# Kernel tuning notes

Measured on AMD Instinct MI355X. Metric: run time of the kernel, lower is better.

The kernel has to match this reference:

```python
import jax, jax.numpy as jnp
import numpy as np

N, B, C, K, FF = 1024, 8, 256, 4, 2048

def layer_norm(x, g, b, eps=1e-5):
    mu = jnp.mean(x, axis=-1, keepdims=True)
    var = jnp.var(x, axis=-1, keepdims=True)
    return (x - mu) / jnp.sqrt(var + eps) * g + b

def setup_inputs() -> dict:
    key = jax.random.key(0)
    ks = jax.random.split(key, 10)
    s = 0.02
    return {
        "src_tokens": jax.random.normal(ks[0], (N, B, C), jnp.float32),
        "matched_token_list": jax.random.normal(ks[1], (K, N, B, C), jnp.float32),
        "pos_embed": jax.random.normal(ks[2], (N, B, C), jnp.float32),
        "mask": jnp.zeros((B, N, N), jnp.float32),
        "W_agg": jax.random.normal(ks[3], (C * K, C), jnp.float32) * s,
        "b_agg": jnp.zeros((C,), jnp.float32),
        "W1": jax.random.normal(ks[4], (C, FF), jnp.float32) * s,
        "b1": jnp.zeros((FF,), jnp.float32),
        "W2": jax.random.normal(ks[5], (FF, C), jnp.float32) * s,
        "b2": jnp.zeros((C,), jnp.float32),
        "g1": jnp.ones((C,), jnp.float32),
        "be1": jnp.zeros((C,), jnp.float32),
        "g2": jnp.ones((C,), jnp.float32),
        "be2": jnp.zeros((C,), jnp.float32),
    }

def reference(src_tokens, matched_token_list, pos_embed, mask,
              W_agg, b_agg, W1, b1, W2, b2, g1, be1, g2, be2):
    # q: (n,b,c) -> (b,n,c); k/v: (K,n,b,c) -> (K,b,n,c)
    q = jnp.transpose(src_tokens + pos_embed, (1, 0, 2))
    k = jnp.transpose(matched_token_list + pos_embed[None], (0, 2, 1, 3))
    v = jnp.transpose(matched_token_list, (0, 2, 1, 3))
    q_scaled = q / jnp.sqrt(jnp.asarray(q.shape[-1], q.dtype))
    # scores: (K,b,n,n) with additive mask bias
    scores = jnp.einsum('bnc,kbmc->kbnm', q_scaled, k) + mask[None]
    attn = jax.nn.softmax(scores, axis=-1)
    out_k = jnp.einsum('kbnm,kbmc->kbnc', attn, v)  # (K,b,n,c)
    # concat over K on channel dim: (b,n,K*c)
    cat = jnp.transpose(out_k, (1, 2, 0, 3)).reshape(q.shape[0], q.shape[1], -1)
    rec = cat @ W_agg + b_agg  # (b,n,c)
    rec = jnp.transpose(rec, (1, 0, 2))  # (n,b,c)
    rec = layer_norm(src_tokens + rec, g1, be1)
    ffn = jax.nn.relu(rec @ W1 + b1) @ W2 + b2
    rec = layer_norm(rec + ffn, g2, be2)
    return rec
```

## Files before the change

### kernel.cpp

```cpp
#include <hip/hip_runtime.h>

#define N_SEQ 1024
#define B_SZ 8
#define C_DIM 256
#define K_HEADS 4
#define FF_DIM 2048

typedef short s16x8 __attribute__((ext_vector_type(8)));
typedef float f32x4v __attribute__((ext_vector_type(4)));

#define GLOAD_LDS16(src, dst)                                                              \
    __builtin_amdgcn_global_load_lds((const __attribute__((address_space(1))) void*)(src), \
                                     (__attribute__((address_space(3))) void*)(dst), 16, 0, 0)

__device__ __forceinline__ unsigned short f2bf(float f) {
    unsigned u = __builtin_bit_cast(unsigned, f);
    u += 0x7FFFu + ((u >> 16) & 1u);
    return (unsigned short)(u >> 16);
}
__device__ __forceinline__ float bf2f(unsigned short h) {
    unsigned u = ((unsigned)h) << 16;
    return __builtin_bit_cast(float, u);
}


__global__ __launch_bounds__(256) void prep_q_kernel(const float* __restrict__ src,
                                                     const float* __restrict__ pos,
                                                     unsigned short* __restrict__ qb) {
    int t = blockIdx.x * 256 + threadIdx.x;
    int i4 = t * 4;
    float4 s = *reinterpret_cast<const float4*>(src + i4);
    float4 p = *reinterpret_cast<const float4*>(pos + i4);
    int n = i4 >> 11;
    int rem = i4 & 2047;
    int b = rem >> 8;
    int c = rem & 255;
    int out = (b * N_SEQ + n) * C_DIM + c;
    *reinterpret_cast<ushort4*>(qb + out) = make_ushort4(
        f2bf((s.x + p.x) * 0.0625f), f2bf((s.y + p.y) * 0.0625f),
        f2bf((s.z + p.z) * 0.0625f), f2bf((s.w + p.w) * 0.0625f));
}

__global__ __launch_bounds__(256) void prep_kv_kernel(const float* __restrict__ matched,
                                                      const float* __restrict__ pos,
                                                      unsigned short* __restrict__ kb,
                                                      unsigned short* __restrict__ vfrag) {
    __shared__ unsigned short Vl[64][256];
    int blk = blockIdx.x;
    int nt = blk & 15, pr = blk >> 4;
    int k = pr >> 3, b = pr & 7;
    int n0 = nt * 64;
    int t = threadIdx.x;
    int c4 = (t & 63) * 4;
#pragma unroll
    for (int r = 0; r < 16; r++) {
        int nl = (t >> 6) * 16 + r;
        int n = n0 + nl;
        size_t mi = ((size_t)(k * N_SEQ + n) * B_SZ + b) * C_DIM + c4;
        float4 m = *reinterpret_cast<const float4*>(matched + mi);
        float4 p = *reinterpret_cast<const float4*>(pos + ((size_t)n * B_SZ + b) * C_DIM + c4);
        *reinterpret_cast<ushort4*>(kb + ((size_t)pr * N_SEQ + n) * C_DIM + c4) =
            make_ushort4(f2bf(m.x + p.x), f2bf(m.y + p.y), f2bf(m.z + p.z), f2bf(m.w + p.w));
        *reinterpret_cast<ushort4*>(&Vl[nl][c4]) =
            make_ushort4(f2bf(m.x), f2bf(m.y), f2bf(m.z), f2bf(m.w));
    }
    __syncthreads();
#pragma unroll
    for (int h = 0; h < 2; h++) {
        unsigned short* tb = vfrag + ((size_t)(pr * 32 + nt * 2 + h)) * 8192;
#pragma unroll
        for (int g = 0; g < 4; g++) {
            int c2 = t + 256 * g;
            int ct = c2 >> 6;
            int lane2 = c2 & 63;
            int l152 = lane2 & 15, lg2 = lane2 >> 4;
            s16x8 v;
#pragma unroll
            for (int e = 0; e < 8; e++)
                v[e] = (short)Vl[h * 32 + lg2 * 8 + e][ct * 16 + l152];
            *reinterpret_cast<s16x8*>(tb + (size_t)c2 * 8) = v;
        }
    }
}

__global__ __launch_bounds__(256) void transpose_all_kernel(const float* __restrict__ Wagg,
                                                            const float* __restrict__ W1,
                                                            const float* __restrict__ W2,
                                                            unsigned short* __restrict__ WaggT,
                                                            unsigned short* __restrict__ W1T,
                                                            unsigned short* __restrict__ W2T) {
    int idx = blockIdx.x * 256 + threadIdx.x;
    if (idx < 262144) {
        int c = idx >> 10, r = idx & 1023;
        WaggT[idx] = f2bf(Wagg[(size_t)r * 256 + c]);
    } else if (idx < 786432) {
        int i = idx - 262144;
        int c = i >> 8, r = i & 255;
        W1T[i] = f2bf(W1[(size_t)r * 2048 + c]);
    } else {
        int i = idx - 786432;
        int c = i >> 11, r = i & 2047;
        W2T[i] = f2bf(W2[(size_t)r * 256 + c]);
    }
}

__global__ __launch_bounds__(256, 2) void attn_kernel(const unsigned short* __restrict__ qb,
                                                      const unsigned short* __restrict__ kb,
                                                      const unsigned short* __restrict__ vfrag,
                                                      const float* __restrict__ mask,
                                                      unsigned short* __restrict__ att) {
    __shared__ unsigned short Kl[2][8192];
    __shared__ unsigned short Psh[2][4][16][40];
    __shared__ float scl[2][4][17];
    __shared__ float lrex[4][17];

    int bx = blockIdx.x;
    int b = bx & 7;
    int r2 = bx >> 3;
    int kidx = r2 & 3;
    int qtb = r2 >> 2;
    int pr = kidx * 8 + b;

    int tid = threadIdx.x, wid = tid >> 6, lane = tid & 63;
    int l15 = lane & 15, lg = lane >> 4;
    int q0 = qtb * 64 + wid * 16;

    s16x8 qf[8];
    const unsigned short* qrow = qb + ((size_t)(b * N_SEQ + q0 + l15)) * C_DIM + lg * 8;
#pragma unroll
    for (int cc = 0; cc < 8; cc++) qf[cc] = *reinterpret_cast<const s16x8*>(qrow + cc * 32);

    f32x4v oacc[16];
#pragma unroll
    for (int i = 0; i < 16; i++) oacc[i] = (f32x4v){0.f, 0.f, 0.f, 0.f};
    float mrun = -3e38f, lrun = 0.f;

    const unsigned short* kbp = kb + (size_t)pr * N_SEQ * C_DIM;
    const unsigned short* vfp = vfrag + (size_t)pr * 32 * 8192 + lane * 8;
    const float* mrow = mask + ((size_t)b * N_SEQ + q0 + l15) * N_SEQ;

    auto stage_k = [&](int kv0, unsigned short* buf) {
#pragma unroll
        for (int i = 0; i < 4; i++) {
            int ch = (wid * 4 + i) * 64 + lane;
            int r = ch >> 5;
            int ce = ((ch & 31) * 8) ^ ((r & 7) << 3);
            GLOAD_LDS16(kbp + (size_t)(kv0 + r) * C_DIM + ce, &buf[(wid * 4 + i) * 512]);
        }
    };

    stage_k(0, &Kl[0][0]);
    f32x4v mc0 = *reinterpret_cast<const f32x4v*>(mrow + lg * 4);
    f32x4v mc1 = *reinterpret_cast<const f32x4v*>(mrow + 16 + lg * 4);

    int swz = (l15 & 7) << 3;
    for (int t = 0; t < 32; t++) {
        int cur = t & 1;
        int kv0 = t * 32;
        __syncthreads();
        if (t + 1 < 32) stage_k(kv0 + 32, &Kl[cur ^ 1][0]);

        const unsigned short* vsrc = vfp + (size_t)t * 8192;
        s16x8 vreg[4];
#pragma unroll
        for (int c = 0; c < 4; c++)
            vreg[c] = *reinterpret_cast<const s16x8*>(vsrc + (wid * 4 + c) * 512);

        f32x4v s0 = {0.f, 0.f, 0.f, 0.f}, s1 = {0.f, 0.f, 0.f, 0.f};
        const unsigned short* KlB = &Kl[cur][0];
        __builtin_amdgcn_s_setprio(1);
#pragma unroll
        for (int cc = 0; cc < 8; cc++) {
            s16x8 k0 = *reinterpret_cast<const s16x8*>(KlB + l15 * 256 + ((cc * 32 + lg * 8) ^ swz));
            s16x8 k1 = *reinterpret_cast<const s16x8*>(KlB + (16 + l15) * 256 + ((cc * 32 + lg * 8) ^ swz));
            s0 = __builtin_amdgcn_mfma_f32_16x16x32_bf16(k0, qf[cc], s0, 0, 0, 0);
            s1 = __builtin_amdgcn_mfma_f32_16x16x32_bf16(k1, qf[cc], s1, 0, 0, 0);
        }
        __builtin_amdgcn_s_setprio(0);
#pragma unroll
        for (int jj = 0; jj < 4; jj++) { s0[jj] += mc0[jj]; s1[jj] += mc1[jj]; }
        if (t + 1 < 32) {
            mc0 = *reinterpret_cast<const f32x4v*>(mrow + kv0 + 32 + lg * 4);
            mc1 = *reinterpret_cast<const f32x4v*>(mrow + kv0 + 48 + lg * 4);
        }

        float pm = fmaxf(fmaxf(fmaxf(s0[0], s0[1]), fmaxf(s0[2], s0[3])),
                         fmaxf(fmaxf(s1[0], s1[1]), fmaxf(s1[2], s1[3])));
        pm = fmaxf(pm, __shfl_xor(pm, 16));
        pm = fmaxf(pm, __shfl_xor(pm, 32));
        float sc = 1.0f;
        if (__any(pm > mrun + 8.f)) {
            float mn = fmaxf(mrun, pm);
            sc = __expf(mrun - mn);
            mrun = mn;
        }
        float p0[4], p1[4];
#pragma unroll
        for (int jj = 0; jj < 4; jj++) {
            p0[jj] = __expf(s0[jj] - mrun);
            p1[jj] = __expf(s1[jj] - mrun);
        }
        float ps = (p0[0] + p0[1]) + (p0[2] + p0[3]) + (p1[0] + p1[1]) + (p1[2] + p1[3]);
        ps += __shfl_xor(ps, 16);
        ps += __shfl_xor(ps, 32);
        lrun = lrun * sc + ps;

        *reinterpret_cast<ushort4*>(&Psh[cur][wid][l15][lg * 4]) =
            make_ushort4(f2bf(p0[0]), f2bf(p0[1]), f2bf(p0[2]), f2bf(p0[3]));
        *reinterpret_cast<ushort4*>(&Psh[cur][wid][l15][16 + lg * 4]) =
            make_ushort4(f2bf(p1[0]), f2bf(p1[1]), f2bf(p1[2]), f2bf(p1[3]));
        if (lane < 16) scl[cur][wid][lane] = sc;
        __syncthreads();

        __builtin_amdgcn_s_setprio(1);
#pragma unroll
        for (int j = 0; j < 4; j++) {
            float scj = scl[cur][j][l15];
            s16x8 pf = *reinterpret_cast<const s16x8*>(&Psh[cur][j][l15][lg * 8]);
            if (__any(scj != 1.0f)) {
#pragma unroll
                for (int c = 0; c < 4; c++)
#pragma unroll
                    for (int jj = 0; jj < 4; jj++) oacc[j * 4 + c][jj] *= scj;
            }
#pragma unroll
            for (int c = 0; c < 4; c++) {
                int idx = j * 4 + c;
                oacc[idx] = __builtin_amdgcn_mfma_f32_16x16x32_bf16(vreg[c], pf, oacc[idx], 0, 0, 0);
            }
        }
        __builtin_amdgcn_s_setprio(0);
    }

    if (lane < 16) lrex[wid][lane] = lrun;
    __syncthreads();
#pragma unroll
    for (int j = 0; j < 4; j++) {
        float invj = 1.0f / lrex[j][l15];
#pragma unroll
        for (int c = 0; c < 4; c++) {
            int idx = j * 4 + c;
            size_t orow = ((size_t)(b * N_SEQ + qtb * 64 + j * 16 + l15)) * (K_HEADS * C_DIM)
                          + kidx * C_DIM + wid * 64 + c * 16 + lg * 4;
            *reinterpret_cast<ushort4*>(att + orow) =
                make_ushort4(f2bf(oacc[idx][0] * invj), f2bf(oacc[idx][1] * invj),
                             f2bf(oacc[idx][2] * invj), f2bf(oacc[idx][3] * invj));
        }
    }
}

template <int BM, int BN, int RELU, int OUTBF, int SPLITK>
__global__ __launch_bounds__(256) void gemm_bt_kernel(const unsigned short* __restrict__ A,
                                                      const unsigned short* __restrict__ Bt,
                                                      const float* __restrict__ bias,
                                                      float* __restrict__ Cf0,
                                                      float* __restrict__ Cf1,
                                                      unsigned short* __restrict__ Cb,
                                                      int M, int Nn, int Kd) {
    constexpr int WAVES_N = (BM == 128) ? 2 : 4;
    constexpr int WN = BN / WAVES_N;
    constexpr int NT = WN / 16;
    constexpr int TILE = (BM + BN) * 64;
    constexpr int CALLS = (BM + BN) / 32;
    __shared__ unsigned short Sl[2][TILE];
    int tm0 = blockIdx.y * BM, tn0 = blockIdx.x * BN;
    int kz = (SPLITK == 2) ? blockIdx.z : 0;
    int kbase = kz * (Kd / SPLITK);
    int tid = threadIdx.x, wid = tid >> 6, lane = tid & 63;
    int l15 = lane & 15, lg = lane >> 4;
    int wm = (wid / WAVES_N) * 64, wn = (wid % WAVES_N) * WN;

    f32x4v acc[4][NT];
#pragma unroll
    for (int i = 0; i < 4; i++)
#pragma unroll
        for (int j = 0; j < NT; j++) acc[i][j] = (f32x4v){0.f, 0.f, 0.f, 0.f};

    auto stage = [&](int k0, unsigned short* buf) {
#pragma unroll
        for (int i = 0; i < CALLS; i++) {
            int chb = (i * 4 + wid) * 64;
            int ch = chb + lane;
            const unsigned short* src;
            if (chb < BM * 8) {
                int r = ch >> 3;
                int c8 = ((ch & 7) * 8) ^ ((r & 7) << 3);
                src = A + (size_t)(tm0 + r) * Kd + k0 + c8;
            } else {
                int ch2 = ch - BM * 8;
                int r = ch2 >> 3;
                int c8 = ((ch2 & 7) * 8) ^ ((r & 7) << 3);
                src = Bt + (size_t)(tn0 + r) * Kd + k0 + c8;
            }
            GLOAD_LDS16(src, buf + chb * 8);
        }
    };

    stage(kbase, &Sl[0][0]);
    int nk = (Kd / SPLITK) >> 6;
    int swz = (l15 & 7) << 3;
    for (int kt = 0; kt < nk; kt++) {
        int cur = kt & 1;
        __syncthreads();
        if (kt + 1 < nk) stage(kbase + (kt + 1) * 64, &Sl[cur ^ 1][0]);
        const unsigned short* SA = &Sl[cur][0];
        const unsigned short* SB = SA + BM * 64;
        s16x8 af[4][2], bf[NT][2];
#pragma unroll
        for (int mt = 0; mt < 4; mt++)
#pragma unroll
            for (int h = 0; h < 2; h++)
                af[mt][h] = *reinterpret_cast<const s16x8*>(
                    SA + (wm + mt * 16 + l15) * 64 + ((h * 32 + lg * 8) ^ swz));
#pragma unroll
        for (int nt = 0; nt < NT; nt++)
#pragma unroll
            for (int h = 0; h < 2; h++)
                bf[nt][h] = *reinterpret_cast<const s16x8*>(
                    SB + (wn + nt * 16 + l15) * 64 + ((h * 32 + lg * 8) ^ swz));
        __builtin_amdgcn_s_setprio(1);
#pragma unroll
        for (int mt = 0; mt < 4; mt++)
#pragma unroll
            for (int nt = 0; nt < NT; nt++) {
                acc[mt][nt] = __builtin_amdgcn_mfma_f32_16x16x32_bf16(af[mt][0], bf[nt][0], acc[mt][nt], 0, 0, 0);
                acc[mt][nt] = __builtin_amdgcn_mfma_f32_16x16x32_bf16(af[mt][1], bf[nt][1], acc[mt][nt], 0, 0, 0);
            }
        __builtin_amdgcn_s_setprio(0);
    }

    float* Cf = (SPLITK == 2 && kz) ? Cf1 : Cf0;
#pragma unroll
    for (int mt = 0; mt < 4; mt++) {
#pragma unroll
        for (int nt = 0; nt < NT; nt++) {
#pragma unroll
            for (int j = 0; j < 4; j++) {
                int row = tm0 + wm + mt * 16 + lg * 4 + j;
                int col = tn0 + wn + nt * 16 + l15;
                float bv = (SPLITK == 2 && kz) ? 0.f : bias[col];
                float v = acc[mt][nt][j] + bv;
                if (RELU) v = fmaxf(v, 0.f);
                if (OUTBF) Cb[(size_t)row * Nn + col] = f2bf(v);
                else       Cf[(size_t)row * Nn + col] = v;
            }
        }
    }
}

__global__ __launch_bounds__(256) void ln1_kernel(const float* __restrict__ src,
                                                  const float* __restrict__ p0,
                                                  const float* __restrict__ p1,
                                                  const float* __restrict__ g,
                                                  const float* __restrict__ be,
                                                  unsigned short* __restrict__ outb) {
    int r = blockIdx.x * 4 + (threadIdx.x >> 6);
    int lane = threadIdx.x & 63;
    int n = r >> 3, b = r & 7;
    int c = lane * 4;
    size_t tb_ = ((size_t)(b * N_SEQ + n)) * C_DIM + c;
    float4 xs = *reinterpret_cast<const float4*>(src + (size_t)r * C_DIM + c);
    float4 xa = *reinterpret_cast<const float4*>(p0 + tb_);
    float4 xb = *reinterpret_cast<const float4*>(p1 + tb_);
    float x[4] = {xs.x + xa.x + xb.x, xs.y + xa.y + xb.y,
                  xs.z + xa.z + xb.z, xs.w + xa.w + xb.w};
    float s = x[0] + x[1] + x[2] + x[3];
    float q = x[0] * x[0] + x[1] * x[1] + x[2] * x[2] + x[3] * x[3];
#pragma unroll
    for (int d = 1; d < 64; d <<= 1) {
        s += __shfl_xor(s, d);
        q += __shfl_xor(q, d);
    }
    float mean = s * (1.f / 256.f);
    float var = q * (1.f / 256.f) - mean * mean;
    float rstd = rsqrtf(var + 1e-5f);
    float4 gv = *reinterpret_cast<const float4*>(g + c);
    float4 bv = *reinterpret_cast<const float4*>(be + c);
    *reinterpret_cast<ushort4*>(outb + (size_t)r * C_DIM + c) = make_ushort4(
        f2bf((x[0] - mean) * rstd * gv.x + bv.x), f2bf((x[1] - mean) * rstd * gv.y + bv.y),
        f2bf((x[2] - mean) * rstd * gv.z + bv.z), f2bf((x[3] - mean) * rstd * gv.w + bv.w));
}

__global__ __launch_bounds__(256) void ln2_kernel(const unsigned short* __restrict__ rec1b,
                                                  const float* __restrict__ p0,
                                                  const float* __restrict__ p1,
                                                  const float* __restrict__ g,
                                                  const float* __restrict__ be,
                                                  float* __restrict__ out) {
    int r = blockIdx.x * 4 + (threadIdx.x >> 6);
    int lane = threadIdx.x & 63;
    int c = lane * 4;
    size_t base = (size_t)r * C_DIM + c;
    ushort4 xr = *reinterpret_cast<const ushort4*>(rec1b + base);
    float4 xa = *reinterpret_cast<const float4*>(p0 + base);
    float4 xb = *reinterpret_cast<const float4*>(p1 + base);
    float x[4] = {bf2f(xr.x) + xa.x + xb.x, bf2f(xr.y) + xa.y + xb.y,
                  bf2f(xr.z) + xa.z + xb.z, bf2f(xr.w) + xa.w + xb.w};
    float s = x[0] + x[1] + x[2] + x[3];
    float q = x[0] * x[0] + x[1] * x[1] + x[2] * x[2] + x[3] * x[3];
#pragma unroll
    for (int d = 1; d < 64; d <<= 1) {
        s += __shfl_xor(s, d);
        q += __shfl_xor(q, d);
    }
    float mean = s * (1.f / 256.f);
    float var = q * (1.f / 256.f) - mean * mean;
    float rstd = rsqrtf(var + 1e-5f);
    float4 gv = *reinterpret_cast<const float4*>(g + c);
    float4 bv = *reinterpret_cast<const float4*>(be + c);
    *reinterpret_cast<float4*>(out + base) = make_float4(
        (x[0] - mean) * rstd * gv.x + bv.x,
        (x[1] - mean) * rstd * gv.y + bv.y,
        (x[2] - mean) * rstd * gv.z + bv.z,
        (x[3] - mean) * rstd * gv.w + bv.w);
}


extern "C" void kernel_launch(void* const* d_in, const int* in_sizes, int n_in,
                              void* d_out, int out_size, void* d_ws, size_t ws_size,
                              hipStream_t stream) {
    const float* src   = (const float*)d_in[0];
    const float* match = (const float*)d_in[1];
    const float* pos   = (const float*)d_in[2];
    const float* mask  = (const float*)d_in[3];
    const float* Wagg  = (const float*)d_in[4];
    const float* bagg  = (const float*)d_in[5];
    const float* W1    = (const float*)d_in[6];
    const float* b1    = (const float*)d_in[7];
    const float* W2    = (const float*)d_in[8];
    const float* b2    = (const float*)d_in[9];
    const float* g1    = (const float*)d_in[10];
    const float* be1   = (const float*)d_in[11];
    const float* g2    = (const float*)d_in[12];
    const float* be2   = (const float*)d_in[13];

    char* ws = (char*)d_ws;
    unsigned short* qb    = (unsigned short*)(ws + 0);
    unsigned short* kb    = (unsigned short*)(ws + 4194304);
    unsigned short* vfrag = (unsigned short*)(ws + 20971520);
    unsigned short* att   = (unsigned short*)(ws + 37748736);
    unsigned short* WaggT = (unsigned short*)(ws + 54525952);
    unsigned short* W1T   = (unsigned short*)(ws + 55050240);
    unsigned short* W2T   = (unsigned short*)(ws + 56098816);
    float*          rec_p0 = (float*)(ws + 57147392);
    float*          rec_p1 = (float*)(ws + 65536000);
    unsigned short* rec1b = (unsigned short*)(ws + 0);
    unsigned short* hid   = (unsigned short*)(ws + 4194304);
    float*          ffn_p0 = rec_p0;
    float*          ffn_p1 = rec_p1;
    float* outp = (float*)d_out;

    prep_q_kernel<<<2048, 256, 0, stream>>>(src, pos, qb);
    prep_kv_kernel<<<512, 256, 0, stream>>>(match, pos, kb, vfrag);
    transpose_all_kernel<<<5120, 256, 0, stream>>>(Wagg, W1, W2, WaggT, W1T, W2T);

    attn_kernel<<<512, 256, 0, stream>>>(qb, kb, vfrag, mask, att);

    gemm_bt_kernel<64, 128, 0, 0, 2><<<dim3(2, 128, 2), 256, 0, stream>>>(
        att, WaggT, bagg, rec_p0, rec_p1, nullptr, B_SZ * N_SEQ, C_DIM, K_HEADS * C_DIM);
    ln1_kernel<<<2048, 256, 0, stream>>>(src, rec_p0, rec_p1, g1, be1, rec1b);
    gemm_bt_kernel<128, 128, 1, 1, 1><<<dim3(16, 64), 256, 0, stream>>>(
        rec1b, W1T, b1, nullptr, nullptr, hid, N_SEQ * B_SZ, FF_DIM, C_DIM);
    gemm_bt_kernel<64, 128, 0, 0, 2><<<dim3(2, 128, 2), 256, 0, stream>>>(
        hid, W2T, b2, ffn_p0, ffn_p1, nullptr, N_SEQ * B_SZ, C_DIM, FF_DIM);
    ln2_kernel<<<2048, 256, 0, stream>>>(rec1b, ffn_p0, ffn_p1, g2, be2, outp);
}
```

Baseline: 145.1 us.

## Split attention KV range across two blocks and merge with a combine kernel

```diff
diff --git a/kernel.cpp b/kernel.cpp
--- a/kernel.cpp
+++ b/kernel.cpp
@@ -104,26 +104,30 @@
     }
 }
 
-__global__ __launch_bounds__(256, 2) void attn_kernel(const unsigned short* __restrict__ qb,
+__global__ __launch_bounds__(256, 4) void attn_kernel(const unsigned short* __restrict__ qb,
                                                       const unsigned short* __restrict__ kb,
                                                       const unsigned short* __restrict__ vfrag,
                                                       const float* __restrict__ mask,
-                                                      unsigned short* __restrict__ att) {
+                                                      unsigned short* __restrict__ op0,
+                                                      unsigned short* __restrict__ op1,
+                                                      float2* __restrict__ mlb) {
     __shared__ unsigned short Kl[2][8192];
-    __shared__ unsigned short Psh[2][4][16][40];
-    __shared__ float scl[2][4][17];
+    __shared__ unsigned short Psh[4][16][40];
+    __shared__ float scl[4][17];
     __shared__ float lrex[4][17];
 
     int bx = blockIdx.x;
     int b = bx & 7;
     int r2 = bx >> 3;
-    int kidx = r2 & 3;
-    int qtb = r2 >> 2;
+    int half = r2 & 1;
+    int kidx = (r2 >> 1) & 3;
+    int qtb = r2 >> 3;
     int pr = kidx * 8 + b;
 
     int tid = threadIdx.x, wid = tid >> 6, lane = tid & 63;
     int l15 = lane & 15, lg = lane >> 4;
     int q0 = qtb * 64 + wid * 16;
+    int kvh = half * 512;
 
     s16x8 qf[8];
     const unsigned short* qrow = qb + ((size_t)(b * N_SEQ + q0 + l15)) * C_DIM + lg * 8;
@@ -135,9 +139,9 @@
     for (int i = 0; i < 16; i++) oacc[i] = (f32x4v){0.f, 0.f, 0.f, 0.f};
     float mrun = -3e38f, lrun = 0.f;
 
-    const unsigned short* kbp = kb + (size_t)pr * N_SEQ * C_DIM;
-    const unsigned short* vfp = vfrag + (size_t)pr * 32 * 8192 + lane * 8;
-    const float* mrow = mask + ((size_t)b * N_SEQ + q0 + l15) * N_SEQ;
+    const unsigned short* kbp = kb + ((size_t)pr * N_SEQ + kvh) * C_DIM;
+    const unsigned short* vfp = vfrag + ((size_t)(pr * 32 + half * 16)) * 8192 + lane * 8;
+    const float* mrow = mask + ((size_t)b * N_SEQ + q0 + l15) * N_SEQ + kvh;
 
     auto stage_k = [&](int kv0, unsigned short* buf) {
 #pragma unroll
@@ -154,11 +158,11 @@
     f32x4v mc1 = *reinterpret_cast<const f32x4v*>(mrow + 16 + lg * 4);
 
     int swz = (l15 & 7) << 3;
-    for (int t = 0; t < 32; t++) {
+    for (int t = 0; t < 16; t++) {
         int cur = t & 1;
         int kv0 = t * 32;
         __syncthreads();
-        if (t + 1 < 32) stage_k(kv0 + 32, &Kl[cur ^ 1][0]);
+        if (t + 1 < 16) stage_k(kv0 + 32, &Kl[cur ^ 1][0]);
 
         const unsigned short* vsrc = vfp + (size_t)t * 8192;
         s16x8 vreg[4];
@@ -179,7 +183,7 @@
         __builtin_amdgcn_s_setprio(0);
 #pragma unroll
         for (int jj = 0; jj < 4; jj++) { s0[jj] += mc0[jj]; s1[jj] += mc1[jj]; }
-        if (t + 1 < 32) {
+        if (t + 1 < 16) {
             mc0 = *reinterpret_cast<const f32x4v*>(mrow + kv0 + 32 + lg * 4);
             mc1 = *reinterpret_cast<const f32x4v*>(mrow + kv0 + 48 + lg * 4);
         }
@@ -205,18 +209,18 @@
         ps += __shfl_xor(ps, 32);
         lrun = lrun * sc + ps;
 
-        *reinterpret_cast<ushort4*>(&Psh[cur][wid][l15][lg * 4]) =
+        *reinterpret_cast<ushort4*>(&Psh[wid][l15][lg * 4]) =
             make_ushort4(f2bf(p0[0]), f2bf(p0[1]), f2bf(p0[2]), f2bf(p0[3]));
-        *reinterpret_cast<ushort4*>(&Psh[cur][wid][l15][16 + lg * 4]) =
+        *reinterpret_cast<ushort4*>(&Psh[wid][l15][16 + lg * 4]) =
             make_ushort4(f2bf(p1[0]), f2bf(p1[1]), f2bf(p1[2]), f2bf(p1[3]));
-        if (lane < 16) scl[cur][wid][lane] = sc;
+        if (lane < 16) scl[wid][lane] = sc;
         __syncthreads();
 
         __builtin_amdgcn_s_setprio(1);
 #pragma unroll
         for (int j = 0; j < 4; j++) {
-            float scj = scl[cur][j][l15];
-            s16x8 pf = *reinterpret_cast<const s16x8*>(&Psh[cur][j][l15][lg * 8]);
+            float scj = scl[j][l15];
+            s16x8 pf = *reinterpret_cast<const s16x8*>(&Psh[j][l15][lg * 8]);
             if (__any(scj != 1.0f)) {
 #pragma unroll
                 for (int c = 0; c < 4; c++)
@@ -234,6 +238,7 @@
 
     if (lane < 16) lrex[wid][lane] = lrun;
     __syncthreads();
+    unsigned short* Op = half ? op1 : op0;
 #pragma unroll
     for (int j = 0; j < 4; j++) {
         float invj = 1.0f / lrex[j][l15];
@@ -242,11 +247,38 @@
             int idx = j * 4 + c;
             size_t orow = ((size_t)(b * N_SEQ + qtb * 64 + j * 16 + l15)) * (K_HEADS * C_DIM)
                           + kidx * C_DIM + wid * 64 + c * 16 + lg * 4;
-            *reinterpret_cast<ushort4*>(att + orow) =
+            *reinterpret_cast<ushort4*>(Op + orow) =
                 make_ushort4(f2bf(oacc[idx][0] * invj), f2bf(oacc[idx][1] * invj),
                              f2bf(oacc[idx][2] * invj), f2bf(oacc[idx][3] * invj));
         }
     }
+    if (lg == 0)
+        mlb[((size_t)(half * 4 + kidx) * 8 + b) * N_SEQ + q0 + l15] = make_float2(mrun, lrun);
+}
+
+__global__ __launch_bounds__(256) void combine_kernel(const unsigned short* __restrict__ op0,
+                                                      const unsigned short* __restrict__ op1,
+                                                      const float2* __restrict__ mlb,
+                                                      unsigned short* __restrict__ att) {
+    int t = blockIdx.x * 256 + threadIdx.x;
+    int kidx = (t >> 5) & 3;
+    int bn = t >> 7;
+    int n = bn & 1023, b = bn >> 10;
+    float2 e0 = mlb[((size_t)kidx * 8 + b) * N_SEQ + n];
+    float2 e1 = mlb[((size_t)(4 + kidx) * 8 + b) * N_SEQ + n];
+    float M = fmaxf(e0.x, e1.x);
+    float w0 = e0.y * __expf(e0.x - M);
+    float w1 = e1.y * __expf(e1.x - M);
+    float r = 1.0f / (w0 + w1);
+    w0 *= r;
+    w1 *= r;
+    s16x8 a = *reinterpret_cast<const s16x8*>(op0 + (size_t)t * 8);
+    s16x8 c = *reinterpret_cast<const s16x8*>(op1 + (size_t)t * 8);
+    s16x8 o;
+#pragma unroll
+    for (int i = 0; i < 8; i++)
+        o[i] = (short)f2bf(w0 * bf2f((unsigned short)a[i]) + w1 * bf2f((unsigned short)c[i]));
+    *reinterpret_cast<s16x8*>(att + (size_t)t * 8) = o;
 }
 
 template <int BM, int BN, int RELU, int OUTBF, int SPLITK>
@@ -444,6 +476,9 @@
     unsigned short* W2T   = (unsigned short*)(ws + 56098816);
     float*          rec_p0 = (float*)(ws + 57147392);
     float*          rec_p1 = (float*)(ws + 65536000);
+    unsigned short* op0   = att;
+    unsigned short* op1   = (unsigned short*)(ws + 57147392);
+    float2*         mlb   = (float2*)(ws + 73924608);
     unsigned short* rec1b = (unsigned short*)(ws + 0);
     unsigned short* hid   = (unsigned short*)(ws + 4194304);
     float*          ffn_p0 = rec_p0;
@@ -454,7 +489,8 @@
     prep_kv_kernel<<<512, 256, 0, stream>>>(match, pos, kb, vfrag);
     transpose_all_kernel<<<5120, 256, 0, stream>>>(Wagg, W1, W2, WaggT, W1T, W2T);
 
-    attn_kernel<<<512, 256, 0, stream>>>(qb, kb, vfrag, mask, att);
+    attn_kernel<<<1024, 256, 0, stream>>>(qb, kb, vfrag, mask, op0, op1, mlb);
+    combine_kernel<<<4096, 256, 0, stream>>>(op0, op1, mlb, att);
 
     gemm_bt_kernel<64, 128, 0, 0, 2><<<dim3(2, 128, 2), 256, 0, stream>>>(
         att, WaggT, bagg, rec_p0, rec_p1, nullptr, B_SZ * N_SEQ, C_DIM, K_HEADS * C_DIM);
```

Result: slower. 248.6 us (+71.3%).
